# Kernel tuning notes

Hardware: AMD Instinct MI355X
Metric: run time of the kernel (lower is better)

The kernel has to match this reference:

```python
import jax, jax.numpy as jnp
import numpy as np
import math

B, T, D = 4, 4096, 1024
H, M = 16, 64
Dh = D // H


def _rope_tables(head_dim, max_seq_len, base=10000):
    inv_freq = 1.0 / (base ** (np.arange(0, head_dim, 2, dtype=np.float32) / head_dim))
    t = np.arange(max_seq_len, dtype=np.float32)
    freqs = np.einsum('i,j->ij', t, inv_freq)  # [T, Dh/2]
    cos = np.cos(freqs)
    sin = np.sin(freqs)
    # interleave (c, c) pairwise -> [T, Dh]
    cos = np.stack((cos, cos), axis=-1).reshape(max_seq_len, head_dim)
    sin = np.stack((sin, sin), axis=-1).reshape(max_seq_len, head_dim)
    return jnp.asarray(cos), jnp.asarray(sin)


def setup_inputs() -> dict:
    key = jax.random.key(0)
    ks = jax.random.split(key, 6)
    s = 1.0 / math.sqrt(D)
    x = jax.random.normal(ks[0], (B, T, D), dtype=jnp.float32)
    Wq = jnp.clip(jax.random.normal(ks[1], (D, D)) * s, -2 * s, 2 * s).astype(jnp.float32)
    Wk = jnp.clip(jax.random.normal(ks[2], (D, D)) * s, -2 * s, 2 * s).astype(jnp.float32)
    Wv = jnp.clip(jax.random.normal(ks[3], (D, D)) * s, -2 * s, 2 * s).astype(jnp.float32)
    Wo = jnp.clip(jax.random.normal(ks[4], (D, D)) * s, -2 * s, 2 * s).astype(jnp.float32)
    latent_code = (jax.random.normal(ks[5], (H, M, Dh)) * 0.02).astype(jnp.float32)
    rope_cos, rope_sin = _rope_tables(Dh, T)
    mask = jnp.ones((B, 1, T, 1), dtype=jnp.int32)
    return {'x': x, 'Wq': Wq, 'Wk': Wk, 'Wv': Wv, 'Wo': Wo,
            'latent_code': latent_code, 'rope_cos': rope_cos,
            'rope_sin': rope_sin, 'mask': mask}


def _rotate(x):
    # (x1, x2) pairs -> (-x2, x1), interleaved
    x2 = x.reshape(*x.shape[:-1], -1, 2)
    return jnp.stack((-x2[..., 1], x2[..., 0]), axis=-1).reshape(x.shape)


def reference(x, Wq, Wk, Wv, Wo, latent_code, rope_cos, rope_sin, mask):
    Bc, Tc, Dc = x.shape
    scale = 1.0 / math.sqrt(Dh)
    # projections -> [B, H, T, Dh]
    q = (x @ Wq.T).reshape(Bc, Tc, H, Dh).transpose(0, 2, 1, 3)
    k = (x @ Wk.T).reshape(Bc, Tc, H, Dh).transpose(0, 2, 1, 3)
    v = (x @ Wv.T).reshape(Bc, Tc, H, Dh).transpose(0, 2, 1, 3)
    cos = rope_cos[:Tc][None, None]  # [1,1,T,Dh]
    sin = rope_sin[:Tc][None, None]
    q = q * cos + _rotate(q) * sin
    k = k * cos + _rotate(k) * sin
    # Stage 1: token -> latent assignment, softmax over tokens (axis=2)
    assign_logits = jnp.einsum('bhtd,hmd->bhtm', k, latent_code) * scale
    assign_logits = jnp.where(mask == 0, -jnp.inf, assign_logits)
    assign = jax.nn.softmax(assign_logits, axis=2)
    k_lat = jnp.einsum('bhtm,bhtd->bhmd', assign, k)
    v_lat = jnp.einsum('bhtm,bhtd->bhmd', assign, v)
    # Stage 2: query attends to latents, softmax over latents (axis=-1)
    att2 = jnp.einsum('bhtd,bhmd->bhtm', q, k_lat) * scale
    p2 = jax.nn.softmax(att2, axis=-1)
    out = jnp.einsum('bhtm,bhmd->bhtd', p2, v_lat)
    out = out.transpose(0, 2, 1, 3).reshape(Bc, Tc, Dc)
    return out @ Wo.T
```

## Files before the change

### kernel.cpp

```cpp
#include <hip/hip_runtime.h>
#include <hip/hip_bf16.h>
#include <stdint.h>


#define DEV static __device__ __forceinline__

using short8 = __attribute__((ext_vector_type(8))) short;
using f32x4  = __attribute__((ext_vector_type(4))) float;

#define ZERO4 (f32x4){0.f, 0.f, 0.f, 0.f}

DEV float bf2f(unsigned short u) {
  union { unsigned int i; float f; } c; c.i = ((unsigned int)u) << 16; return c.f;
}
DEV unsigned short f2bf(float f) {
  __hip_bfloat16 h = __float2bfloat16(f);
  unsigned short u; __builtin_memcpy(&u, &h, 2); return u;
}
DEV f32x4 mfma16(short8 a, short8 b, f32x4 c) {
  return __builtin_amdgcn_mfma_f32_16x16x32_bf16(a, b, c, 0, 0, 0);
}
#define GLOAD_LDS16(G, L) __builtin_amdgcn_global_load_lds( \
    (const __attribute__((address_space(1))) void*)(G),     \
    (__attribute__((address_space(3))) void*)(L), 16, 0, 0)

__global__ void cvt_bf16(const float* __restrict__ src,
                         __hip_bfloat16* __restrict__ dst, int n) {
  int i = (blockIdx.x * blockDim.x + threadIdx.x) * 4;
  if (i >= n) return;
  const float4 v = *(const float4*)(src + i);
  ushort4 o;
  o.x = f2bf(v.x); o.y = f2bf(v.y); o.z = f2bf(v.z); o.w = f2bf(v.w);
  *(ushort4*)(dst + i) = o;
}

template<int MODE, int ROPE>
__global__ __launch_bounds__(512, 2)
void gemm256(const __hip_bfloat16* __restrict__ A,
             const __hip_bfloat16* __restrict__ Bt,
             void* __restrict__ Cout, __hip_bfloat16* __restrict__ Ct,
             const float* __restrict__ cosT, const float* __restrict__ sinT,
             int M, int N, int K) {
  __shared__ __hip_bfloat16 As[2][256 * 64];
  __shared__ __hip_bfloat16 Bs[2][256 * 64];
  const int tid = threadIdx.x;
  const int w = tid >> 6, l = tid & 63;
  const int lr = l & 15, lg = l >> 4;
  const int rowA0 = blockIdx.x * 256;
  const int colB0 = blockIdx.y * 256;
  const int srow = w * 8 + (l >> 3);
  const int skk  = (((l & 7) ^ (l >> 3)) * 8);
  const __hip_bfloat16* Ab = A  + (size_t)(rowA0 + srow) * K + skk;
  const __hip_bfloat16* Bb = Bt + (size_t)(colB0 + srow) * K + skk;
  f32x4 acc[8][4];
#pragma unroll
  for (int i = 0; i < 8; ++i)
#pragma unroll
    for (int j = 0; j < 4; ++j) acc[i][j] = ZERO4;
  const int wr = (w >> 2) * 128;
  const int wc = (w & 3) * 64;
  const int NT = K >> 6;

#define G_STAGE(kt, buf)                                                          \
  {                                                                               \
    const int k0s = (kt) * 64;                                                    \
    _Pragma("unroll")                                                             \
    for (int i = 0; i < 4; ++i) {                                                 \
      GLOAD_LDS16(Ab + (size_t)(i * 64) * K + k0s, &As[buf][i * 4096 + w * 512]); \
      GLOAD_LDS16(Bb + (size_t)(i * 64) * K + k0s, &Bs[buf][i * 4096 + w * 512]); \
    }                                                                             \
  }

  G_STAGE(0, 0);
  for (int kt = 0; kt < NT; ++kt) {
    const int cur = kt & 1;
    if (kt + 1 < NT) {
      G_STAGE(kt + 1, cur ^ 1);
      asm volatile("s_waitcnt vmcnt(8)" ::: "memory");
    } else {
      asm volatile("s_waitcnt vmcnt(0)" ::: "memory");
    }
    __builtin_amdgcn_s_barrier();
    __builtin_amdgcn_s_setprio(1);
#pragma unroll
    for (int s = 0; s < 2; ++s) {
      short8 fa[8], fb[4];
#pragma unroll
      for (int i = 0; i < 8; ++i)
        fa[i] = *(const short8*)&As[cur][(wr + i * 16 + lr) * 64 +
                                         (((s * 4 + lg) ^ (lr & 7)) * 8)];
#pragma unroll
      for (int j = 0; j < 4; ++j)
        fb[j] = *(const short8*)&Bs[cur][(wc + j * 16 + lr) * 64 +
                                         (((s * 4 + lg) ^ (lr & 7)) * 8)];
#pragma unroll
      for (int i = 0; i < 8; ++i)
#pragma unroll
        for (int j = 0; j < 4; ++j)
          acc[i][j] = mfma16(fa[i], fb[j], acc[i][j]);
    }
    __builtin_amdgcn_s_setprio(0);
    __builtin_amdgcn_s_barrier();
  }
#undef G_STAGE

  const int r0 = rowA0 + wr + lg * 4;
  const int c0 = colB0 + wc + lr;
  if (ROPE) {
#pragma unroll
    for (int i = 0; i < 8; ++i)
#pragma unroll
      for (int j = 0; j < 4; ++j)
#pragma unroll
        for (int r = 0; r < 4; ++r) {
          const int m = r0 + i * 16 + r;
          const int n = c0 + j * 16;
          const int t = m & 4095, d = n & 63;
          const float c = cosT[t * 64 + d];
          const float s = sinT[t * 64 + d];
          const float v = acc[i][j][r];
          const float other = __shfl_xor(v, 1, 64);
          acc[i][j][r] = v * c + ((n & 1) ? other : -other) * s;
        }
  }
  if (MODE <= 2) {
#pragma unroll
    for (int i = 0; i < 8; ++i)
#pragma unroll
      for (int j = 0; j < 4; ++j)
#pragma unroll
        for (int r = 0; r < 4; ++r) {
          const size_t idx = (size_t)(r0 + i * 16 + r) * N + (c0 + j * 16);
          if (MODE == 0) ((float*)Cout)[idx] = acc[i][j][r];
          else ((__hip_bfloat16*)Cout)[idx] = __float2bfloat16(acc[i][j][r]);
        }
  }
  if (MODE >= 2) {
#pragma unroll
    for (int i = 0; i < 8; ++i)
#pragma unroll
      for (int j = 0; j < 4; ++j) {
        const int m0 = r0 + i * 16;
        const int n  = c0 + j * 16;
        const size_t row = (size_t)(((m0 >> 12) * 16 + (n >> 6)) * 64 + (n & 63));
        ushort4 pk;
        pk.x = f2bf(acc[i][j][0]); pk.y = f2bf(acc[i][j][1]);
        pk.z = f2bf(acc[i][j][2]); pk.w = f2bf(acc[i][j][3]);
        *(ushort4*)&Ct[row * 4096 + (m0 & 4095)] = pk;
      }
  }
}

__global__ __launch_bounds__(256)
void stage1_logits(const __hip_bfloat16* __restrict__ kmat,
                   const float* __restrict__ latent,
                   const int* __restrict__ mask,
                   __hip_bfloat16* __restrict__ S,
                   float* __restrict__ pmax, float* __restrict__ psum) {
  const int bh = blockIdx.x, chunk = blockIdx.y;
  const int b = bh >> 4, h = bh & 15;
  const int tid = threadIdx.x, w = tid >> 6, l = tid & 63;
  const int lr = l & 15, lg = l >> 4;
  short8 la[4][2];
#pragma unroll
  for (int n = 0; n < 4; ++n)
#pragma unroll
    for (int s = 0; s < 2; ++s) {
      const float* lp = &latent[((size_t)h * 64 + n * 16 + lr) * 64 + s * 32 + lg * 8];
      short8 f;
#pragma unroll
      for (int j = 0; j < 8; ++j) f[j] = (short)f2bf(lp[j]);
      la[n][s] = f;
    }
  float mx[16], sm[16];
#pragma unroll
  for (int i = 0; i < 16; ++i) { mx[i] = -3.0e38f; sm[i] = 0.f; }
  for (int tile = 0; tile < 8; ++tile) {
    const int t = chunk * 512 + tile * 64 + w * 16 + lr;
    const __hip_bfloat16* kp = &kmat[((size_t)(b * 4096 + t) * 16 + h) * 64 + lg * 8];
    const short8 kb0 = *(const short8*)kp;
    const short8 kb1 = *(const short8*)(kp + 32);
    const bool live = (mask[b * 4096 + t] != 0);
    f32x4 acc[4];
#pragma unroll
    for (int n = 0; n < 4; ++n) {
      acc[n] = ZERO4;
      acc[n] = mfma16(la[n][0], kb0, acc[n]);
      acc[n] = mfma16(la[n][1], kb1, acc[n]);
    }
#pragma unroll
    for (int n = 0; n < 4; ++n)
#pragma unroll
      for (int r = 0; r < 4; ++r) {
        const float v = acc[n][r] * 0.125f;
        const int m = n * 16 + lg * 4 + r;
        unsigned short sv = live ? f2bf(v) : (unsigned short)0xFF80;
        ((unsigned short*)S)[((size_t)bh * 64 + m) * 4096 + t] = sv;
        if (live) {
          const int idx = n * 4 + r;
          const float nm = fmaxf(mx[idx], v);
          sm[idx] = sm[idx] * __expf(mx[idx] - nm) + __expf(v - nm);
          mx[idx] = nm;
        }
      }
  }
#pragma unroll
  for (int o = 1; o < 16; o <<= 1)
#pragma unroll
    for (int i = 0; i < 16; ++i) {
      const float omx = __shfl_xor(mx[i], o, 64);
      const float osm = __shfl_xor(sm[i], o, 64);
      const float nm = fmaxf(mx[i], omx);
      sm[i] = sm[i] * __expf(mx[i] - nm) + osm * __expf(omx - nm);
      mx[i] = nm;
    }
  if (lr == 0) {
    const size_t pb = ((size_t)(bh * 8 + chunk) * 4 + w) * 64;
#pragma unroll
    for (int n = 0; n < 4; ++n)
#pragma unroll
      for (int r = 0; r < 4; ++r) {
        const int m = n * 16 + lg * 4 + r;
        pmax[pb + m] = mx[n * 4 + r];
        psum[pb + m] = sm[n * 4 + r];
      }
  }
}

__global__ void stage1_reduce(const float* __restrict__ pmax,
                              const float* __restrict__ psum,
                              float* __restrict__ cmax, float* __restrict__ cinv) {
  const int i = blockIdx.x * 256 + threadIdx.x;
  if (i >= 4096) return;
  const int bh = i >> 6, m = i & 63;
  float mx = -3.0e38f;
#pragma unroll
  for (int c = 0; c < 32; ++c)
    mx = fmaxf(mx, pmax[((size_t)bh * 32 + c) * 64 + m]);
  float sm = 0.f;
#pragma unroll
  for (int c = 0; c < 32; ++c)
    sm += psum[((size_t)bh * 32 + c) * 64 + m] *
          __expf(pmax[((size_t)bh * 32 + c) * 64 + m] - mx);
  cmax[i] = mx;
  cinv[i] = 1.f / sm;
}

__global__ __launch_bounds__(256)
void latgemm5(const __hip_bfloat16* __restrict__ S,
              const __hip_bfloat16* __restrict__ kT,
              const __hip_bfloat16* __restrict__ vT,
              const float* __restrict__ cmax, const float* __restrict__ cinv,
              float* __restrict__ partials) {
  const int bh = blockIdx.x;
  const int tid = threadIdx.x, w = tid >> 6, l = tid & 63;
  const int slice = blockIdx.y * 4 + w;
  const int lr = l & 15;
  const int lk = (l >> 4) * 8;
  const size_t base = (size_t)bh * 64 * 4096;
  float cm[4], ci[4];
#pragma unroll
  for (int i = 0; i < 4; ++i) {
    cm[i] = cmax[bh * 64 + i * 16 + lr];
    ci[i] = cinv[bh * 64 + i * 16 + lr];
  }
  f32x4 ak[4][4], av[4][4];
#pragma unroll
  for (int i = 0; i < 4; ++i)
#pragma unroll
    for (int j = 0; j < 4; ++j) { ak[i][j] = ZERO4; av[i][j] = ZERO4; }
  for (int ks = 0; ks < 8; ++ks) {
    const int t = slice * 256 + ks * 32 + lk;
    short8 fp[4], fk[4], fv[4];
#pragma unroll
    for (int i = 0; i < 4; ++i) {
      const size_t ro = base + (size_t)(i * 16 + lr) * 4096 + t;
      const short8 sv = *(const short8*)&S[ro];
      short8 p;
#pragma unroll
      for (int j = 0; j < 8; ++j)
        p[j] = (short)f2bf(__expf(bf2f((unsigned short)sv[j]) - cm[i]) * ci[i]);
      fp[i] = p;
      fk[i] = *(const short8*)&kT[ro];
      fv[i] = *(const short8*)&vT[ro];
    }
#pragma unroll
    for (int i = 0; i < 4; ++i)
#pragma unroll
      for (int j = 0; j < 4; ++j) {
        ak[i][j] = mfma16(fp[i], fk[j], ak[i][j]);
        av[i][j] = mfma16(fv[i], fp[j], av[i][j]);
      }
  }
  float* pk = partials + ((size_t)(slice * 64 + bh)) * 8192;
#pragma unroll
  for (int i = 0; i < 4; ++i)
#pragma unroll
    for (int j = 0; j < 4; ++j)
#pragma unroll
      for (int r = 0; r < 4; ++r) {
        const int row = i * 16 + 4 * (l >> 4) + r;
        const int col = j * 16 + lr;
        pk[(size_t)row * 64 + col]        = ak[i][j][r];
        pk[4096 + (size_t)row * 64 + col] = av[i][j][r];
      }
}

__global__ void latreduce(const float* __restrict__ partials,
                          __hip_bfloat16* __restrict__ k_lat,
                          __hip_bfloat16* __restrict__ v_latT) {
  const int i = blockIdx.x * 256 + threadIdx.x;
  const int bh = i >> 13, off = i & 8191;
  float sm = 0.f;
#pragma unroll
  for (int c = 0; c < 16; ++c)
    sm += partials[((size_t)(c * 64 + bh)) * 8192 + off];
  if (off < 4096) k_lat[(size_t)bh * 4096 + off] = __float2bfloat16(sm);
  else            v_latT[(size_t)bh * 4096 + (off - 4096)] = __float2bfloat16(sm);
}

__global__ __launch_bounds__(256)
void stage2_attn(const __hip_bfloat16* __restrict__ q,
                 const __hip_bfloat16* __restrict__ k_lat,
                 const __hip_bfloat16* __restrict__ v_latT,
                 __hip_bfloat16* __restrict__ attn) {
  __shared__ unsigned short Pl[4][16][64];
  const int bid = blockIdx.x;
  const int bh = bid >> 6, tt = (bid & 63) * 64;
  const int b = bh >> 4, h = bh & 15;
  const int tid = threadIdx.x, w = tid >> 6, l = tid & 63;
  const size_t qoff = ((size_t)(b * 4096 + tt + w * 16 + (l & 15)) * 16 + h) * 64;
  const short8 a0 = *(const short8*)&q[qoff + (l >> 4) * 8];
  const short8 a1 = *(const short8*)&q[qoff + 32 + (l >> 4) * 8];
  f32x4 att[4];
#pragma unroll
  for (int n = 0; n < 4; ++n) att[n] = ZERO4;
#pragma unroll
  for (int n = 0; n < 4; ++n) {
    const __hip_bfloat16* kl = &k_lat[((size_t)bh * 64 + n * 16 + (l & 15)) * 64];
    const short8 b0 = *(const short8*)&kl[(l >> 4) * 8];
    const short8 b1 = *(const short8*)&kl[32 + (l >> 4) * 8];
    att[n] = mfma16(a0, b0, att[n]);
    att[n] = mfma16(a1, b1, att[n]);
  }
  float p[4][4];
#pragma unroll
  for (int r = 0; r < 4; ++r) {
    const float v0 = att[0][r] * 0.125f, v1 = att[1][r] * 0.125f;
    const float v2 = att[2][r] * 0.125f, v3 = att[3][r] * 0.125f;
    float mxv = fmaxf(fmaxf(v0, v1), fmaxf(v2, v3));
#pragma unroll
    for (int o = 1; o < 16; o <<= 1) mxv = fmaxf(mxv, __shfl_xor(mxv, o, 64));
    const float e0 = __expf(v0 - mxv), e1 = __expf(v1 - mxv);
    const float e2 = __expf(v2 - mxv), e3 = __expf(v3 - mxv);
    float sum = e0 + e1 + e2 + e3;
#pragma unroll
    for (int o = 1; o < 16; o <<= 1) sum += __shfl_xor(sum, o, 64);
    const float inv = 1.f / sum;
    p[0][r] = e0 * inv; p[1][r] = e1 * inv; p[2][r] = e2 * inv; p[3][r] = e3 * inv;
  }
#pragma unroll
  for (int n = 0; n < 4; ++n)
#pragma unroll
    for (int r = 0; r < 4; ++r) {
      const int row = 4 * (l >> 4) + r;
      const int col = n * 16 + (l & 15);
      Pl[w][row][col ^ ((row & 7) << 3)] = f2bf(p[n][r]);
    }
  __syncthreads();
  const int arow = l & 15;
  const short8 pa0 = *(const short8*)&Pl[w][arow][(((l >> 4) + 0) ^ (arow & 7)) * 8];
  const short8 pa1 = *(const short8*)&Pl[w][arow][(((l >> 4) + 4) ^ (arow & 7)) * 8];
  f32x4 ov[4];
#pragma unroll
  for (int n = 0; n < 4; ++n) ov[n] = ZERO4;
#pragma unroll
  for (int n = 0; n < 4; ++n) {
    const __hip_bfloat16* vt = &v_latT[((size_t)bh * 64 + n * 16 + (l & 15)) * 64];
    const short8 b0 = *(const short8*)&vt[(l >> 4) * 8];
    const short8 b1 = *(const short8*)&vt[32 + (l >> 4) * 8];
    ov[n] = mfma16(pa0, b0, ov[n]);
    ov[n] = mfma16(pa1, b1, ov[n]);
  }
#pragma unroll
  for (int n = 0; n < 4; ++n) {
    const int d = n * 16 + (l & 15);
#pragma unroll
    for (int r = 0; r < 4; ++r) {
      const int trow = tt + w * 16 + 4 * (l >> 4) + r;
      attn[((size_t)(b * 4096 + trow) * 16 + h) * 64 + d] = __float2bfloat16(ov[n][r]);
    }
  }
}

extern "C" void kernel_launch(void* const* d_in, const int* in_sizes, int n_in,
                              void* d_out, int out_size, void* d_ws, size_t ws_size,
                              hipStream_t stream) {
  const float* x      = (const float*)d_in[0];
  const float* Wq     = (const float*)d_in[1];
  const float* Wk     = (const float*)d_in[2];
  const float* Wv     = (const float*)d_in[3];
  const float* Wo     = (const float*)d_in[4];
  const float* latent = (const float*)d_in[5];
  const float* cosT   = (const float*)d_in[6];
  const float* sinT   = (const float*)d_in[7];
  const int*   mask   = (const int*)d_in[8];

  char* ws = (char*)d_ws;
  __hip_bfloat16* xb = (__hip_bfloat16*)ws;
  __hip_bfloat16* Wb = (__hip_bfloat16*)(ws + 33554432);
  __hip_bfloat16* qb = (__hip_bfloat16*)(ws + 41943040);
  __hip_bfloat16* kb = (__hip_bfloat16*)(ws + 75497472);
  __hip_bfloat16* kT = (__hip_bfloat16*)(ws + 109051904);
  __hip_bfloat16* vT = (__hip_bfloat16*)(ws + 142606336);
  char* tail = ws + 176160768;
  float* pmax = (float*)tail;
  float* psum = pmax + 131072;
  float* cmax = psum + 131072;
  float* cinv = cmax + 4096;
  __hip_bfloat16* k_lat  = (__hip_bfloat16*)(cinv + 4096);
  __hip_bfloat16* v_latT = k_lat + 262144;

  __hip_bfloat16* S    = xb;
  __hip_bfloat16* attn = qb;
  float* partials = (float*)kb;

  cvt_bf16<<<16384, 256, 0, stream>>>(x, xb, 16777216);
  cvt_bf16<<<1024, 256, 0, stream>>>(Wq, Wb + 0 * 1048576, 1048576);
  cvt_bf16<<<1024, 256, 0, stream>>>(Wk, Wb + 1 * 1048576, 1048576);
  cvt_bf16<<<1024, 256, 0, stream>>>(Wv, Wb + 2 * 1048576, 1048576);
  cvt_bf16<<<1024, 256, 0, stream>>>(Wo, Wb + 3 * 1048576, 1048576);

  dim3 gg(64, 4);
  gemm256<1, 1><<<gg, 512, 0, stream>>>(xb, Wb + 0 * 1048576, qb, nullptr, cosT, sinT, 16384, 1024, 1024);
  gemm256<2, 1><<<gg, 512, 0, stream>>>(xb, Wb + 1 * 1048576, kb, kT, cosT, sinT, 16384, 1024, 1024);
  gemm256<3, 0><<<gg, 512, 0, stream>>>(xb, Wb + 2 * 1048576, nullptr, vT, nullptr, nullptr, 16384, 1024, 1024);

  dim3 sg(64, 8);
  stage1_logits<<<sg, 256, 0, stream>>>(kb, latent, mask, S, pmax, psum);
  stage1_reduce<<<16, 256, 0, stream>>>(pmax, psum, cmax, cinv);

  dim3 lg(64, 4);
  latgemm5<<<lg, 256, 0, stream>>>(S, kT, vT, cmax, cinv, partials);
  latreduce<<<2048, 256, 0, stream>>>(partials, k_lat, v_latT);

  stage2_attn<<<4096, 256, 0, stream>>>(qb, k_lat, v_latT, attn);
  gemm256<0, 0><<<gg, 512, 0, stream>>>(attn, Wb + 3 * 1048576, d_out, nullptr, nullptr, nullptr, 16384, 1024, 1024);
}
```

Baseline: 321.9 us.

## Restructure GEMM main loop into fine-grained phased pipeline with split A/B staging

Replaces the simple double-buffered K loop with an 8-phase schedule over two K tiles per iteration. Global-to-LDS loads for A and B are split into half-tile chunks and interleaved between fragment reads and MFMA groups, with a barrier between phases. The aim is to overlap memory traffic with MFMA work more evenly, in the style of ping-pong schedules. It adds many more barriers and assumes NT is even, and the buffer reuse timing is delicate.

```diff
diff --git a/kernel.cpp b/kernel.cpp
--- a/kernel.cpp
+++ b/kernel.cpp
@@ -60,49 +60,89 @@
   const int wr = (w >> 2) * 128;
   const int wc = (w & 3) * 64;
   const int NT = K >> 6;
-
-#define G_STAGE(kt, buf)                                                          \
-  {                                                                               \
-    const int k0s = (kt) * 64;                                                    \
-    _Pragma("unroll")                                                             \
-    for (int i = 0; i < 4; ++i) {                                                 \
-      GLOAD_LDS16(Ab + (size_t)(i * 64) * K + k0s, &As[buf][i * 4096 + w * 512]); \
-      GLOAD_LDS16(Bb + (size_t)(i * 64) * K + k0s, &Bs[buf][i * 4096 + w * 512]); \
-    }                                                                             \
-  }
-
-  G_STAGE(0, 0);
-  for (int kt = 0; kt < NT; ++kt) {
-    const int cur = kt & 1;
-    if (kt + 1 < NT) {
-      G_STAGE(kt + 1, cur ^ 1);
-      asm volatile("s_waitcnt vmcnt(8)" ::: "memory");
-    } else {
-      asm volatile("s_waitcnt vmcnt(0)" ::: "memory");
-    }
-    __builtin_amdgcn_s_barrier();
-    __builtin_amdgcn_s_setprio(1);
-#pragma unroll
-    for (int s = 0; s < 2; ++s) {
-      short8 fa[8], fb[4];
-#pragma unroll
-      for (int i = 0; i < 8; ++i)
-        fa[i] = *(const short8*)&As[cur][(wr + i * 16 + lr) * 64 +
-                                         (((s * 4 + lg) ^ (lr & 7)) * 8)];
-#pragma unroll
-      for (int j = 0; j < 4; ++j)
-        fb[j] = *(const short8*)&Bs[cur][(wc + j * 16 + lr) * 64 +
-                                         (((s * 4 + lg) ^ (lr & 7)) * 8)];
-#pragma unroll
-      for (int i = 0; i < 8; ++i)
-#pragma unroll
-        for (int j = 0; j < 4; ++j)
-          acc[i][j] = mfma16(fa[i], fb[j], acc[i][j]);
-    }
-    __builtin_amdgcn_s_setprio(0);
-    __builtin_amdgcn_s_barrier();
-  }
-#undef G_STAGE
+  const int NI = NT >> 1;
+
+#define STAGE_A(kt, h)                                                           \
+  if ((kt) < NT) {                                                               \
+    const size_t go = (size_t)((h) * 128) * K + (size_t)(kt) * 64;               \
+    GLOAD_LDS16(Ab + go,                &As[(kt) & 1][((h) * 128 + w * 8) * 64]); \
+    GLOAD_LDS16(Ab + go + (size_t)64 * K, &As[(kt) & 1][((h) * 128 + 64 + w * 8) * 64]); \
+  }
+#define STAGE_B(kt, h)                                                           \
+  if ((kt) < NT) {                                                               \
+    const size_t go = (size_t)((h) * 128) * K + (size_t)(kt) * 64;               \
+    GLOAD_LDS16(Bb + go,                &Bs[(kt) & 1][((h) * 128 + w * 8) * 64]); \
+    GLOAD_LDS16(Bb + go + (size_t)64 * K, &Bs[(kt) & 1][((h) * 128 + 64 + w * 8) * 64]); \
+  }
+#define READ_FRAGS(buf, s, FA, FB)                                               \
+  {                                                                              \
+    _Pragma("unroll")                                                            \
+    for (int i = 0; i < 8; ++i)                                                  \
+      FA[i] = *(const short8*)&As[buf][(wr + i * 16 + lr) * 64 +                 \
+                                       ((((s) * 4 + lg) ^ (lr & 7)) * 8)];       \
+    _Pragma("unroll")                                                            \
+    for (int j = 0; j < 4; ++j)                                                  \
+      FB[j] = *(const short8*)&Bs[buf][(wc + j * 16 + lr) * 64 +                 \
+                                       ((((s) * 4 + lg) ^ (lr & 7)) * 8)];       \
+  }
+#define MM(FA, FB, j0)                                                           \
+  {                                                                              \
+    __builtin_amdgcn_s_setprio(1);                                               \
+    _Pragma("unroll")                                                            \
+    for (int i = 0; i < 8; ++i) {                                                \
+      acc[i][j0] = mfma16(FA[i], FB[j0], acc[i][j0]);                            \
+      acc[i][j0 + 1] = mfma16(FA[i], FB[j0 + 1], acc[i][j0 + 1]);                \
+    }                                                                            \
+    __builtin_amdgcn_s_setprio(0);                                               \
+  }
+#define PH_SYNC                                                                  \
+  asm volatile("s_waitcnt lgkmcnt(0)" ::: "memory");                             \
+  __builtin_amdgcn_s_barrier();                                                  \
+  asm volatile("" ::: "memory");
+
+  STAGE_A(0, 0); STAGE_A(0, 1); STAGE_B(0, 0); STAGE_B(0, 1);
+  STAGE_A(1, 0); STAGE_A(1, 1);
+
+  for (int it = 0; it < NI; ++it) {
+    const int k0 = 2 * it, k1 = 2 * it + 1;
+    short8 fa0[8], fb0[4], fa1[8], fb1[4];
+    asm volatile("s_waitcnt vmcnt(4)" ::: "memory");
+    PH_SYNC;
+    READ_FRAGS(0, 0, fa0, fb0);
+    STAGE_B(k1, 0);
+    MM(fa0, fb0, 0);
+    PH_SYNC;
+    READ_FRAGS(0, 1, fa1, fb1);
+    STAGE_B(k1, 1);
+    MM(fa0, fb0, 2);
+    PH_SYNC;
+    STAGE_A(k0 + 2, 0);
+    MM(fa1, fb1, 0);
+    PH_SYNC;
+    STAGE_A(k0 + 2, 1);
+    MM(fa1, fb1, 2);
+    if (it + 1 < NI) { asm volatile("s_waitcnt vmcnt(4)" ::: "memory"); }
+    else             { asm volatile("s_waitcnt vmcnt(0)" ::: "memory"); }
+    PH_SYNC;
+    READ_FRAGS(1, 0, fa0, fb0);
+    STAGE_B(k0 + 2, 0);
+    MM(fa0, fb0, 0);
+    PH_SYNC;
+    READ_FRAGS(1, 1, fa1, fb1);
+    STAGE_B(k0 + 2, 1);
+    MM(fa0, fb0, 2);
+    PH_SYNC;
+    STAGE_A(k0 + 3, 0);
+    MM(fa1, fb1, 0);
+    PH_SYNC;
+    STAGE_A(k0 + 3, 1);
+    MM(fa1, fb1, 2);
+  }
+#undef STAGE_A
+#undef STAGE_B
+#undef READ_FRAGS
+#undef MM
+#undef PH_SYNC
 
   const int r0 = rowA0 + wr + lg * 4;
   const int c0 = colB0 + wc + lr;
```

After: 419.0 us. 30.2% more time.

## Merge conversion launches, fold stage1 reduce into latent GEMM, halve its grid

Applied to the files above, without the earlier changes.

Five fp32-to-bf16 conversion launches become one kernel that picks its source by block index. The max/sum reduction of stage1 is now computed per block in shared memory inside the latent GEMM, which removes the separate reduce kernel and its cmax/cinv buffers. The latent GEMM grid drops from 4 to 2 y-blocks, each wave covering 512 tokens, so latreduce sums 8 partials instead of 16. This cuts launches and partial-sum traffic, but gives the GEMM only 128 blocks, so occupancy falls and each block repeats the small reduction.

```diff
diff --git a/kernel.cpp b/kernel.cpp
--- a/kernel.cpp
+++ b/kernel.cpp
@@ -24,10 +24,24 @@
     (const __attribute__((address_space(1))) void*)(G),     \
     (__attribute__((address_space(3))) void*)(L), 16, 0, 0)
 
-__global__ void cvt_bf16(const float* __restrict__ src,
-                         __hip_bfloat16* __restrict__ dst, int n) {
-  int i = (blockIdx.x * blockDim.x + threadIdx.x) * 4;
-  if (i >= n) return;
+__global__ void cvt_all(const float* __restrict__ x,
+                        const float* __restrict__ Wq, const float* __restrict__ Wk,
+                        const float* __restrict__ Wv, const float* __restrict__ Wo,
+                        __hip_bfloat16* __restrict__ xb,
+                        __hip_bfloat16* __restrict__ Wb) {
+  const int bid = blockIdx.x;
+  const float* src;
+  __hip_bfloat16* dst;
+  int base;
+  if (bid < 16384) {
+    src = x; dst = xb; base = bid;
+  } else {
+    const int k = (bid - 16384) >> 10;
+    src = (k == 0) ? Wq : (k == 1) ? Wk : (k == 2) ? Wv : Wo;
+    dst = Wb + (size_t)k * 1048576;
+    base = (bid - 16384) & 1023;
+  }
+  const int i = (base * 256 + threadIdx.x) * 4;
   const float4 v = *(const float4*)(src + i);
   ushort4 o;
   o.x = f2bf(v.x); o.y = f2bf(v.y); o.z = f2bf(v.z); o.w = f2bf(v.w);
@@ -227,50 +241,46 @@
   }
 }
 
-__global__ void stage1_reduce(const float* __restrict__ pmax,
-                              const float* __restrict__ psum,
-                              float* __restrict__ cmax, float* __restrict__ cinv) {
-  const int i = blockIdx.x * 256 + threadIdx.x;
-  if (i >= 4096) return;
-  const int bh = i >> 6, m = i & 63;
-  float mx = -3.0e38f;
-#pragma unroll
-  for (int c = 0; c < 32; ++c)
-    mx = fmaxf(mx, pmax[((size_t)bh * 32 + c) * 64 + m]);
-  float sm = 0.f;
-#pragma unroll
-  for (int c = 0; c < 32; ++c)
-    sm += psum[((size_t)bh * 32 + c) * 64 + m] *
-          __expf(pmax[((size_t)bh * 32 + c) * 64 + m] - mx);
-  cmax[i] = mx;
-  cinv[i] = 1.f / sm;
-}
-
 __global__ __launch_bounds__(256)
-void latgemm5(const __hip_bfloat16* __restrict__ S,
+void latgemm6(const __hip_bfloat16* __restrict__ S,
               const __hip_bfloat16* __restrict__ kT,
               const __hip_bfloat16* __restrict__ vT,
-              const float* __restrict__ cmax, const float* __restrict__ cinv,
+              const float* __restrict__ pmax, const float* __restrict__ psum,
               float* __restrict__ partials) {
+  __shared__ float scm[64], sci[64];
   const int bh = blockIdx.x;
   const int tid = threadIdx.x, w = tid >> 6, l = tid & 63;
   const int slice = blockIdx.y * 4 + w;
   const int lr = l & 15;
   const int lk = (l >> 4) * 8;
   const size_t base = (size_t)bh * 64 * 4096;
+  if (tid < 64) {
+    float mxv = -3.0e38f;
+#pragma unroll
+    for (int c = 0; c < 32; ++c)
+      mxv = fmaxf(mxv, pmax[((size_t)bh * 32 + c) * 64 + tid]);
+    float smv = 0.f;
+#pragma unroll
+    for (int c = 0; c < 32; ++c)
+      smv += psum[((size_t)bh * 32 + c) * 64 + tid] *
+             __expf(pmax[((size_t)bh * 32 + c) * 64 + tid] - mxv);
+    scm[tid] = mxv;
+    sci[tid] = 1.f / smv;
+  }
+  __syncthreads();
   float cm[4], ci[4];
 #pragma unroll
   for (int i = 0; i < 4; ++i) {
-    cm[i] = cmax[bh * 64 + i * 16 + lr];
-    ci[i] = cinv[bh * 64 + i * 16 + lr];
+    cm[i] = scm[i * 16 + lr];
+    ci[i] = sci[i * 16 + lr];
   }
   f32x4 ak[4][4], av[4][4];
 #pragma unroll
   for (int i = 0; i < 4; ++i)
 #pragma unroll
     for (int j = 0; j < 4; ++j) { ak[i][j] = ZERO4; av[i][j] = ZERO4; }
-  for (int ks = 0; ks < 8; ++ks) {
-    const int t = slice * 256 + ks * 32 + lk;
+  for (int ks = 0; ks < 16; ++ks) {
+    const int t = slice * 512 + ks * 32 + lk;
     short8 fp[4], fk[4], fv[4];
 #pragma unroll
     for (int i = 0; i < 4; ++i) {
@@ -313,7 +323,7 @@
   const int bh = i >> 13, off = i & 8191;
   float sm = 0.f;
 #pragma unroll
-  for (int c = 0; c < 16; ++c)
+  for (int c = 0; c < 8; ++c)
     sm += partials[((size_t)(c * 64 + bh)) * 8192 + off];
   if (off < 4096) k_lat[(size_t)bh * 4096 + off] = __float2bfloat16(sm);
   else            v_latT[(size_t)bh * 4096 + (off - 4096)] = __float2bfloat16(sm);
@@ -416,20 +426,14 @@
   char* tail = ws + 176160768;
   float* pmax = (float*)tail;
   float* psum = pmax + 131072;
-  float* cmax = psum + 131072;
-  float* cinv = cmax + 4096;
-  __hip_bfloat16* k_lat  = (__hip_bfloat16*)(cinv + 4096);
+  __hip_bfloat16* k_lat  = (__hip_bfloat16*)(psum + 131072);
   __hip_bfloat16* v_latT = k_lat + 262144;
 
   __hip_bfloat16* S    = xb;
   __hip_bfloat16* attn = qb;
   float* partials = (float*)kb;
 
-  cvt_bf16<<<16384, 256, 0, stream>>>(x, xb, 16777216);
-  cvt_bf16<<<1024, 256, 0, stream>>>(Wq, Wb + 0 * 1048576, 1048576);
-  cvt_bf16<<<1024, 256, 0, stream>>>(Wk, Wb + 1 * 1048576, 1048576);
-  cvt_bf16<<<1024, 256, 0, stream>>>(Wv, Wb + 2 * 1048576, 1048576);
-  cvt_bf16<<<1024, 256, 0, stream>>>(Wo, Wb + 3 * 1048576, 1048576);
+  cvt_all<<<20480, 256, 0, stream>>>(x, Wq, Wk, Wv, Wo, xb, Wb);
 
   dim3 gg(64, 4);
   gemm256<1, 1><<<gg, 512, 0, stream>>>(xb, Wb + 0 * 1048576, qb, nullptr, cosT, sinT, 16384, 1024, 1024);
@@ -438,10 +442,9 @@
 
   dim3 sg(64, 8);
   stage1_logits<<<sg, 256, 0, stream>>>(kb, latent, mask, S, pmax, psum);
-  stage1_reduce<<<16, 256, 0, stream>>>(pmax, psum, cmax, cinv);
-
-  dim3 lg(64, 4);
-  latgemm5<<<lg, 256, 0, stream>>>(S, kT, vT, cmax, cinv, partials);
+
+  dim3 lg(64, 2);
+  latgemm6<<<lg, 256, 0, stream>>>(S, kT, vT, pmax, psum, partials);
   latreduce<<<2048, 256, 0, stream>>>(partials, k_lat, v_latT);
 
   stage2_attn<<<4096, 256, 0, stream>>>(qb, k_lat, v_latT, attn);
```

Result: faster. 312.8 us (-2.8%).
